# Performance work log

Hardware: AMD Instinct MI355X
Metric: run time of the kernel (lower is better)

## Reference

```python
import jax, jax.numpy as jnp
import numpy as np

B, LQ, D, H, NL, NP, DFF = 8, 1800, 256, 8, 4, 4, 1024
DH = D // H
SHAPES = np.array([[100, 150], [50, 75], [25, 38], [13, 19]], dtype=np.int64)
LIN = int((SHAPES[:, 0] * SHAPES[:, 1]).sum())
QN, QP = -8.0, 7.0  # 4-bit signed LSQ


def lsq(w, alpha):
    """LSQ weight quantization (per-tensor scale, STE round/grad-scale)."""
    g = 1.0 / jnp.sqrt(w.size * QP)
    a = alpha * g + jax.lax.stop_gradient(alpha - alpha * g)  # grad-scaled alpha
    wn = jnp.clip(w / a, QN, QP)
    wq = wn + jax.lax.stop_gradient(jnp.round(wn) - wn)       # round with STE
    return wq * a


def linear_q(x, w, b, a):
    return x @ lsq(w, a).T + b


def layer_norm(x, g, b, eps=1e-5):
    m = x.mean(-1, keepdims=True)
    v = ((x - m) ** 2).mean(-1, keepdims=True)
    return (x - m) / jnp.sqrt(v + eps) * g + b


def setup_inputs():
    key = jax.random.key(0)
    ks = list(jax.random.split(key, 20))

    def nrm(i, shape, s=0.02):
        return jax.random.normal(ks[i], shape, jnp.float32) * s

    def alpha(w):
        return 2.0 * jnp.mean(jnp.abs(w)) / jnp.sqrt(QP)

    qW, kW, vW, oW = nrm(0, (D, D)), nrm(1, (D, D)), nrm(2, (D, D)), nrm(3, (D, D))
    val_W = nrm(4, (D, D))
    off_W = nrm(5, (H * NL * NP * 2, D))
    aw_W = nrm(6, (H * NL * NP, D))
    out_W = nrm(7, (D, D))
    W1, W2 = nrm(8, (DFF, D)), nrm(9, (D, DFF))
    lsi = np.concatenate([[0], np.cumsum(SHAPES[:, 0] * SHAPES[:, 1])[:-1]]).astype(np.int64)
    z = jnp.zeros
    return dict(
        tgt=nrm(10, (B, LQ, D), 1.0),
        query_pos=nrm(11, (B, LQ, D), 1.0),
        reference_points=jax.random.uniform(ks[12], (B, LQ, NL, 2), jnp.float32),
        src=nrm(13, (B, LIN, D), 1.0),
        qW=qW, qb=z(D), kW=kW, kb=z(D), vW=vW, vb=z(D), oW=oW, ob=z(D),
        a_q=alpha(qW), a_k=alpha(kW), a_v=alpha(vW), a_o=alpha(oW),
        val_W=val_W, val_b=z(D), a_val=alpha(val_W),
        off_W=off_W, off_b=z(H * NL * NP * 2),
        aw_W=aw_W, aw_b=z(H * NL * NP),
        out_W=out_W, out_b=z(D), a_out=alpha(out_W),
        W1=W1, b1=z(DFF), a_w1=alpha(W1),
        W2=W2, b2=z(D), a_w2=alpha(W2),
        ln1_g=jnp.ones(D), ln1_b=z(D),
        ln2_g=jnp.ones(D), ln2_b=z(D),
        ln3_g=jnp.ones(D), ln3_b=z(D),
        src_spatial_shapes=jnp.asarray(SHAPES),
        level_start_index=jnp.asarray(lsi),
        src_padding_mask=jnp.zeros((B, LIN), dtype=bool),
    )


def reference(tgt, query_pos, reference_points, src,
              qW, qb, kW, kb, vW, vb, oW, ob, a_q, a_k, a_v, a_o,
              val_W, val_b, a_val, off_W, off_b, aw_W, aw_b, out_W, out_b, a_out,
              W1, b1, a_w1, W2, b2, a_w2,
              ln1_g, ln1_b, ln2_g, ln2_b, ln3_g, ln3_b,
              src_spatial_shapes, level_start_index, src_padding_mask):
    shapes = np.asarray(src_spatial_shapes)  # static spatial shapes per level

    # ---- quantized self-attention (dropout = eval mode, i.e. identity) ----
    qk_in = tgt + query_pos
    q = linear_q(qk_in, qW, qb, a_q).reshape(B, LQ, H, DH)
    k = linear_q(qk_in, kW, kb, a_k).reshape(B, LQ, H, DH)
    v = linear_q(tgt, vW, vb, a_v).reshape(B, LQ, H, DH)
    scores = jnp.einsum('bqhd,bkhd->bhqk', q, k) / jnp.sqrt(jnp.float32(DH))
    p = jax.nn.softmax(scores, axis=-1)
    sa = jnp.einsum('bhqk,bkhd->bqhd', p, v).reshape(B, LQ, D)
    tgt = layer_norm(tgt + linear_q(sa, oW, ob, a_o), ln2_g, ln2_b)

    # ---- quantized multi-scale deformable cross-attention ----
    query = tgt + query_pos
    value = linear_q(src, val_W, val_b, a_val)
    value = jnp.where(src_padding_mask[..., None], 0.0, value)
    value = value.reshape(B, LIN, H, DH)
    offs = (query @ off_W.T + off_b).reshape(B, LQ, H, NL, NP, 2)
    aw = (query @ aw_W.T + aw_b).reshape(B, LQ, H, NL * NP)
    aw = jax.nn.softmax(aw, axis=-1).reshape(B, LQ, H, NL, NP)
    # offset normalizer is (W_l, H_l)
    norm = jnp.asarray(shapes[:, ::-1].astype(np.float32))  # [NL, 2]
    loc = reference_points[:, :, None, :, None, :] + offs / norm[None, None, None, :, None, :]

    bidx = jnp.arange(B)[:, None, None, None]
    hidx = jnp.arange(H)[None, None, :, None]
    acc = jnp.zeros((B, LQ, H, DH), jnp.float32)
    start = 0
    for l in range(NL):
        Hl, Wl = int(shapes[l, 0]), int(shapes[l, 1])
        v_l = jax.lax.dynamic_slice_in_dim(value, start, Hl * Wl, 1).reshape(B, Hl, Wl, H, DH)
        # grid_sample semantics: align_corners=False, zero padding
        x = loc[:, :, :, l, :, 0] * Wl - 0.5  # [B, LQ, H, NP]
        y = loc[:, :, :, l, :, 1] * Hl - 0.5
        x0 = jnp.floor(x); y0 = jnp.floor(y)
        x0i = x0.astype(jnp.int32); y0i = y0.astype(jnp.int32)
        wx1 = x - x0; wy1 = y - y0
        wx0 = 1.0 - wx1; wy0 = 1.0 - wy1

        def gather(yi, xi):
            valid = (yi >= 0) & (yi < Hl) & (xi >= 0) & (xi < Wl)
            yc = jnp.clip(yi, 0, Hl - 1); xc = jnp.clip(xi, 0, Wl - 1)
            g = v_l[bidx, yc, xc, hidx]  # [B, LQ, H, NP, DH]
            return g * valid[..., None]

        samp = (gather(y0i, x0i) * (wy0 * wx0)[..., None]
                + gather(y0i, x0i + 1) * (wy0 * wx1)[..., None]
                + gather(y0i + 1, x0i) * (wy1 * wx0)[..., None]
                + gather(y0i + 1, x0i + 1) * (wy1 * wx1)[..., None])
        acc = acc + (aw[:, :, :, l, :, None] * samp).sum(axis=3)
        start += Hl * Wl

    ca = linear_q(acc.reshape(B, LQ, D), out_W, out_b, a_out)
    tgt = layer_norm(tgt + ca, ln1_g, ln1_b)

    # ---- quantized FFN ----
    t2 = linear_q(jax.nn.relu(linear_q(tgt, W1, b1, a_w1)), W2, b2, a_w2)
    tgt = layer_norm(tgt + t2, ln3_g, ln3_b)
    return tgt
```

## Files before the change

kernel.cpp:

```cpp
#include <hip/hip_runtime.h>
#include <hip/hip_bf16.h>

static constexpr int B_   = 8;
static constexpr int LQ_  = 1800;
static constexpr int D_   = 256;
static constexpr int H_   = 8;
static constexpr int DFF_ = 1024;
static constexpr int LIN_ = 19947;
static constexpr int MQ_  = B_ * LQ_;
static constexpr int NELEM_ = MQ_ * D_;

#define CDIV(a, b) (((a) + (b) - 1) / (b))

typedef unsigned short u16;
typedef unsigned int   u32;
typedef unsigned long long u64;
typedef __attribute__((ext_vector_type(8))) __bf16 bf16x8;
typedef __attribute__((ext_vector_type(4))) float  f32x4;
typedef __attribute__((ext_vector_type(4))) u32    u32x4;

#if __has_builtin(__builtin_amdgcn_exp2f)
#define EXP2(x) __builtin_amdgcn_exp2f(x)
#else
#define EXP2(x) exp2f(x)
#endif

__device__ __forceinline__ u16 f2bf(float f) {
    union { __bf16 h; u16 u; } v; v.h = (__bf16)f; return v.u;
}
__device__ __forceinline__ float bf2f(u16 u) {
    union { u32 u; float f; } v; v.u = ((u32)u) << 16;
    return v.f;
}

__device__ __forceinline__ f32x4 mfma_bf16(bf16x8 a, bf16x8 b, f32x4 c) {
    return __builtin_amdgcn_mfma_f32_16x16x32_bf16(a, b, c, 0, 0, 0);
}

__device__ __forceinline__ void gload16(const void* g, void* l) {
    __builtin_amdgcn_global_load_lds(
        (const __attribute__((address_space(1))) void*)g,
        (__attribute__((address_space(3))) void*)l,
        16, 0, 0);
}

template <int N> __device__ __forceinline__ void waitvm() {
    if constexpr (N == 0) asm volatile("s_waitcnt vmcnt(0)" ::: "memory");
    else if constexpr (N == 3) asm volatile("s_waitcnt vmcnt(3)" ::: "memory");
    else if constexpr (N == 4) asm volatile("s_waitcnt vmcnt(4)" ::: "memory");
    else if constexpr (N == 5) asm volatile("s_waitcnt vmcnt(5)" ::: "memory");
    else if constexpr (N == 6) asm volatile("s_waitcnt vmcnt(6)" ::: "memory");
}

__global__ void k_prep(
    const float* __restrict__ qW,   const float* __restrict__ kW,
    const float* __restrict__ vW,   const float* __restrict__ oW,
    const float* __restrict__ valW, const float* __restrict__ outW,
    const float* __restrict__ W1,   const float* __restrict__ W2,
    const float* __restrict__ offW, const float* __restrict__ awW,
    const float* __restrict__ a_q,  const float* __restrict__ a_k,
    const float* __restrict__ a_v,  const float* __restrict__ a_o,
    const float* __restrict__ a_val,const float* __restrict__ a_out,
    const float* __restrict__ a_w1, const float* __restrict__ a_w2,
    const float* __restrict__ qb,   const float* __restrict__ kb,
    const float* __restrict__ off_b,const float* __restrict__ aw_b,
    u16* __restrict__ wout, float* __restrict__ bout)
{
    int i = blockIdx.x * 256 + threadIdx.x;
    auto q8 = [&](const float* w, const float* al, int off) {
        float a = al[0];
        float wn = fminf(fmaxf(w[off] / a, -8.f), 7.f);
        wout[i] = f2bf(rintf(wn) * a);
    };
    if      (i <   65536) q8(qW,   a_q,   i);
    else if (i <  131072) q8(kW,   a_k,   i -   65536);
    else if (i <  196608) q8(vW,   a_v,   i -  131072);
    else if (i <  262144) q8(oW,   a_o,   i -  196608);
    else if (i <  327680) q8(valW, a_val, i -  262144);
    else if (i <  393216) q8(outW, a_out, i -  327680);
    else if (i <  655360) q8(W1,   a_w1,  i -  393216);
    else if (i <  917504) q8(W2,   a_w2,  i -  655360);
    else if (i <  983040) wout[i] = f2bf(offW[i - 917504]);
    else if (i < 1015808) wout[i] = f2bf(awW[i - 983040]);
    else if (i < 1016320) { int j = i - 1015808; bout[j]       = (j < 256) ? qb[j]    : kb[j - 256];  }
    else if (i < 1016704) { int j = i - 1016320; bout[512 + j] = (j < 256) ? off_b[j] : aw_b[j - 256]; }
}

__global__ void k_tgtprep(const float* __restrict__ tgt, const float* __restrict__ qpos,
                          u16* __restrict__ A, u16* __restrict__ Bb, int n) {
    int i = blockIdx.x * blockDim.x + threadIdx.x;
    if (i < n) { float t = tgt[i]; A[i] = f2bf(t + qpos[i]); Bb[i] = f2bf(t); }
}

__global__ void k_addcvt2(const u16* __restrict__ a, const float* __restrict__ b,
                          u16* __restrict__ o, int n) {
    int i = blockIdx.x * blockDim.x + threadIdx.x;
    if (i < n) o[i] = f2bf(bf2f(a[i]) + b[i]);
}

__device__ __forceinline__ void storey(float* p, float v) { *p = v; }
__device__ __forceinline__ void storey(u16* p, float v)   { *p = f2bf(v); }

template <typename XT, typename OT, bool RELU, int BN>
__global__ __launch_bounds__(256) void k_gemm3(
    const XT* __restrict__ X, const u16* __restrict__ W,
    const float* __restrict__ bias, OT* __restrict__ Y,
    int M, int N, int K)
{
    constexpr int WN  = BN / 2;
    constexpr int NFR = WN / 16;
    constexpr bool XF32 = (sizeof(XT) == 4);
    constexpr int L = (XF32 ? 2 : 1) + BN / 64;
    constexpr int ASZ = 64 * 32 * (XF32 ? 2 : 1);
    constexpr int BSZ = BN * 32;
    __shared__ __align__(16) u16 As[2][ASZ];
    __shared__ __align__(16) u16 Bs[2][BSZ];

    const int tid = threadIdx.x;
    const int wave = tid >> 6, lane = tid & 63;
    const int wr = wave >> 1, wc = wave & 1;
    const int fr = lane & 15, fg = lane >> 4;
    const int bm = blockIdx.x * 64, bn = blockIdx.y * BN;

    f32x4 acc[2][NFR];
    #pragma unroll
    for (int m = 0; m < 2; ++m)
        #pragma unroll
        for (int n = 0; n < NFR; ++n) acc[m][n] = (f32x4){0.f, 0.f, 0.f, 0.f};

    auto stageA = [&](int buf, int kt) {
        if constexpr (!XF32) {
            int r = (wave << 4) + (lane >> 2);
            int grow = bm + r; if (grow > M - 1) grow = M - 1;
            int cs = (lane & 3) ^ ((lane >> 3) & 3);
            gload16((const u16*)X + (size_t)grow * K + (kt << 5) + (cs << 3),
                    &As[buf][wave * 512]);
        } else {
            float* Af = (float*)As[buf];
            #pragma unroll
            for (int t = 0; t < 2; ++t) {
                int r = (t << 5) + (wave << 3) + (lane >> 3);
                int grow = bm + r; if (grow > M - 1) grow = M - 1;
                int cs = (lane & 7) ^ ((lane >> 3) & 7);
                gload16((const float*)X + (size_t)grow * K + (kt << 5) + (cs << 2),
                        &Af[((t << 5) + (wave << 3)) * 32]);
            }
        }
    };
    auto stageB = [&](int buf, int kt) {
        #pragma unroll
        for (int t = 0; t < BN / 64; ++t) {
            int r = (t << 6) + (wave << 4) + (lane >> 2);
            int cs = (lane & 3) ^ ((lane >> 3) & 3);
            gload16(W + (size_t)(bn + r) * K + (kt << 5) + (cs << 3),
                    &Bs[buf][((t << 6) + (wave << 4)) * 32]);
        }
    };

    stageA(0, 0); stageB(0, 0);

    const int nk = K >> 5;
    int cur = 0;
    for (int kt = 0; kt < nk; ++kt) {
        if (kt + 1 < nk) {
            stageA(cur ^ 1, kt + 1); stageB(cur ^ 1, kt + 1);
            waitvm<L>();
        } else {
            waitvm<0>();
        }
        __builtin_amdgcn_s_barrier();

        bf16x8 af[2], bg[NFR];
        #pragma unroll
        for (int m = 0; m < 2; ++m) {
            int r = wr * 32 + m * 16 + fr;
            if constexpr (!XF32) {
                af[m] = *(const bf16x8*)&As[cur][r * 32 + ((fg ^ ((fr >> 1) & 3)) << 3)];
            } else {
                const float* Af = (const float*)As[cur];
                int s0 = (fg << 1) ^ (fr & 7);
                f32x4 x0 = *(const f32x4*)&Af[r * 32 + (s0 << 2)];
                f32x4 x1 = *(const f32x4*)&Af[r * 32 + ((s0 ^ 1) << 2)];
                #pragma unroll
                for (int j = 0; j < 4; ++j) {
                    af[m][j]     = (__bf16)x0[j];
                    af[m][4 + j] = (__bf16)x1[j];
                }
            }
        }
        #pragma unroll
        for (int n = 0; n < NFR; ++n) {
            int r = wc * WN + n * 16 + fr;
            bg[n] = *(const bf16x8*)&Bs[cur][r * 32 + ((fg ^ ((fr >> 1) & 3)) << 3)];
        }
        #pragma unroll
        for (int m = 0; m < 2; ++m)
            #pragma unroll
            for (int n = 0; n < NFR; ++n)
                acc[m][n] = mfma_bf16(af[m], bg[n], acc[m][n]);

        __builtin_amdgcn_s_barrier();
        cur ^= 1;
    }

    #pragma unroll
    for (int m = 0; m < 2; ++m) {
        #pragma unroll
        for (int i = 0; i < 4; ++i) {
            int grow = bm + wr * 32 + m * 16 + fg * 4 + i;
            if (grow >= M) continue;
            #pragma unroll
            for (int n = 0; n < NFR; ++n) {
                int gcol = bn + wc * WN + n * 16 + fr;
                float v = acc[m][n][i] + bias[gcol];
                if (RELU) v = fmaxf(v, 0.f);
                storey(Y + (size_t)grow * N + gcol, v);
            }
        }
    }
}

__global__ __launch_bounds__(256) void k_attn(
    const u16* __restrict__ QK, const u16* __restrict__ V, u16* __restrict__ O)
{
    __shared__ u16 Ks[128 * 40];
    __shared__ u16 Vt[32 * 136];
    const int b = blockIdx.z, h = blockIdx.y;
    const int q0 = blockIdx.x * 64;
    const int tid = threadIdx.x;
    const int wave = tid >> 6, lane = tid & 63;
    const int fr = lane & 15, fg = lane >> 4;
    constexpr float C2 = 0.25503486f;

    int qg = q0 + wave * 16 + fr; if (qg >= LQ_) qg = LQ_ - 1;
    bf16x8 qf;
    {
        bf16x8 qraw = *(const bf16x8*)&QK[((size_t)(b * LQ_ + qg)) * 512 + h * 32 + fg * 8];
        #pragma unroll
        for (int j = 0; j < 8; ++j) qf[j] = (__bf16)((float)qraw[j] * C2);
    }

    const bf16x8 ones = {(__bf16)1.f, (__bf16)1.f, (__bf16)1.f, (__bf16)1.f,
                         (__bf16)1.f, (__bf16)1.f, (__bf16)1.f, (__bf16)1.f};

    f32x4 o0 = (f32x4){0.f,0.f,0.f,0.f}, o1 = (f32x4){0.f,0.f,0.f,0.f};
    f32x4 lacc = (f32x4){0.f,0.f,0.f,0.f};

    const int kr = tid >> 1, kc = (tid & 1) * 16;
    const int vp = lane, vdh = wave * 8;
    const int cp = ((vp >> 4) << 4) | (((vp >> 1) & 3) << 2) | (((vp >> 3) & 1) << 1) | (vp & 1);

    for (int kb0 = 0; kb0 < LQ_; kb0 += 128) {
        const bool tail = (kb0 + 128 > LQ_);
        __syncthreads();
        {
            int kg = kb0 + kr; if (kg >= LQ_) kg = LQ_ - 1;
            const u16* kp = &QK[((size_t)(b * LQ_ + kg)) * 512 + 256 + h * 32 + kc];
            *(bf16x8*)&Ks[kr * 40 + kc]     = *(const bf16x8*)kp;
            *(bf16x8*)&Ks[kr * 40 + kc + 8] = *(const bf16x8*)(kp + 8);
            int v0 = kb0 + 2 * vp, v1 = v0 + 1;
            if (v0 >= LQ_) v0 = LQ_ - 1;
            if (v1 >= LQ_) v1 = LQ_ - 1;
            union { bf16x8 v; u16 s[8]; } va, vb2;
            va.v  = *(const bf16x8*)&V[((size_t)(b * LQ_ + v0)) * 256 + h * 32 + vdh];
            vb2.v = *(const bf16x8*)&V[((size_t)(b * LQ_ + v1)) * 256 + h * 32 + vdh];
            #pragma unroll
            for (int j = 0; j < 8; ++j)
                *(u32*)&Vt[(vdh + j) * 136 + 2 * cp] = (u32)va.s[j] | ((u32)vb2.s[j] << 16);
        }
        __syncthreads();

        u32x4 pq[4];
        #pragma unroll
        for (int f = 0; f < 8; ++f) {
            bf16x8 ka = *(const bf16x8*)&Ks[(f * 16 + fr) * 40 + fg * 8];
            f32x4 s = mfma_bf16(ka, qf, (f32x4){0.f,0.f,0.f,0.f});
            if (tail) {
                #pragma unroll
                for (int i = 0; i < 4; ++i)
                    if (kb0 + f * 16 + fg * 4 + i >= LQ_) s[i] = -3e38f;
            }
            float p0 = EXP2(s[0]), p1 = EXP2(s[1]);
            float p2 = EXP2(s[2]), p3 = EXP2(s[3]);
            union { __bf16 h[2]; u32 w; } c0, c1;
            c0.h[0] = (__bf16)p0; c0.h[1] = (__bf16)p1;
            c1.h[0] = (__bf16)p2; c1.h[1] = (__bf16)p3;
            pq[f >> 1][(f & 1) * 2 + 0] = c0.w;
            pq[f >> 1][(f & 1) * 2 + 1] = c1.w;
        }

        #pragma unroll
        for (int ks = 0; ks < 4; ++ks) {
            bf16x8 pb  = __builtin_bit_cast(bf16x8, pq[ks]);
            bf16x8 va0 = *(const bf16x8*)&Vt[fr * 136 + ks * 32 + fg * 8];
            bf16x8 va1 = *(const bf16x8*)&Vt[(16 + fr) * 136 + ks * 32 + fg * 8];
            o0 = mfma_bf16(va0, pb, o0);
            o1 = mfma_bf16(va1, pb, o1);
            lacc = mfma_bf16(ones, pb, lacc);
        }
    }

    float inv = 1.f / lacc[0];
    int qout = q0 + wave * 16 + fr;
    if (qout < LQ_) {
        size_t base = ((size_t)(b * LQ_ + qout)) * 256 + h * 32;
        #pragma unroll
        for (int i = 0; i < 4; ++i) {
            O[base + fg * 4 + i]      = f2bf(o0[i] * inv);
            O[base + 16 + fg * 4 + i] = f2bf(o1[i] * inv);
        }
    }
}

__device__ __forceinline__ float ldf(const float* p) { return *p; }
__device__ __forceinline__ float ldf(const u16* p)   { return bf2f(*p); }

template <typename RT, typename OT>
__global__ __launch_bounds__(256) void k_resln(
    const u16* __restrict__ X, const RT* __restrict__ R,
    const float* __restrict__ g, const float* __restrict__ bb,
    OT* __restrict__ O)
{
    const int row = blockIdx.x;
    const int d = threadIdx.x;
    const size_t off = (size_t)row * D_ + d;
    float v = ldf(R + off) + bf2f(X[off]);
    __shared__ float r1[4], r2[4];
    int lane = d & 63, wid = d >> 6;
    float s = v;
    #pragma unroll
    for (int o_ = 32; o_ >= 1; o_ >>= 1) s += __shfl_xor(s, o_);
    if (lane == 0) r1[wid] = s;
    __syncthreads();
    float mean = (r1[0] + r1[1] + r1[2] + r1[3]) * (1.f / 256.f);
    float dv = v - mean;
    float sq = dv * dv;
    #pragma unroll
    for (int o_ = 32; o_ >= 1; o_ >>= 1) sq += __shfl_xor(sq, o_);
    if (lane == 0) r2[wid] = sq;
    __syncthreads();
    float var = (r2[0] + r2[1] + r2[2] + r2[3]) * (1.f / 256.f);
    storey(O + off, dv / sqrtf(var + 1e-5f) * g[d] + bb[d]);
}

__global__ __launch_bounds__(256) void k_sample(
    const float* __restrict__ oaw,
    const u16* __restrict__ value, const float* __restrict__ refp,
    u16* __restrict__ acc_out)
{
    __shared__ u32 pts[2][128][8];
    const int t = threadIdx.x;
    const int bq0 = blockIdx.x * 2;
    const int b = bq0 / LQ_;

    constexpr int Hl[4] = {100, 50, 25, 13};
    constexpr int Wl[4] = {150, 75, 38, 19};
    constexpr int LS[4] = {0, 15000, 18750, 19700};

    {
        const int qsub = t >> 7;
        const int pt = t & 127;
        const int h = pt >> 4, lp = pt & 15;
        const int l = lp >> 2, p = lp & 3;
        const int bq = bq0 + qsub;

        float2 oxy = *(const float2*)&oaw[(size_t)bq * 384 + h * 32 + l * 8 + p * 2];
        float av = oaw[(size_t)bq * 384 + 256 + h * 16 + lp];
        float mx = av;
        #pragma unroll
        for (int s = 1; s < 16; s <<= 1) mx = fmaxf(mx, __shfl_xor(mx, s));
        float e = __expf(av - mx);
        float sum = e;
        #pragma unroll
        for (int s = 1; s < 16; s <<= 1) sum += __shfl_xor(sum, s);
        float a = e / sum;

        float2 rxy = *(const float2*)&refp[(size_t)bq * 8 + l * 2];
        const float Wf = (float)Wl[l], Hf = (float)Hl[l];
        float x = (rxy.x + oxy.x / Wf) * Wf - 0.5f;
        float y = (rxy.y + oxy.y / Hf) * Hf - 0.5f;
        float x0f = floorf(x), y0f = floorf(y);
        int x0 = (int)x0f, y0 = (int)y0f;
        float wx1 = x - x0f, wy1 = y - y0f;
        float wx0 = 1.f - wx1, wy0 = 1.f - wy1;

        u32 ov[4]; float wv[4];
        #pragma unroll
        for (int c = 0; c < 4; ++c) {
            int cy = c >> 1, cx = c & 1;
            int yi = y0 + cy, xi = x0 + cx;
            bool valid = (yi >= 0) && (yi < Hl[l]) && (xi >= 0) && (xi < Wl[l]);
            ov[c] = valid ? (u32)((LS[l] + yi * Wl[l] + xi) * 256 + h * 32) : 0u;
            float w = (cy ? wy1 : wy0) * (cx ? wx1 : wx0) * a;
            wv[c] = valid ? w : 0.f;
        }
        u32* dst = pts[qsub][lp * 8 + h];
        *(uint4*)dst = make_uint4(ov[0], ov[1], ov[2], ov[3]);
        float4 wq = make_float4(wv[0], wv[1], wv[2], wv[3]);
        *(float4*)(dst + 4) = wq;
    }
    __syncthreads();

    const int qsub = t >> 7;
    const int h = (t >> 4) & 7;
    const int dp = t & 15;
    const u16* vb = value + (size_t)b * LIN_ * 256 + 2 * dp;
    float a0 = 0.f, a1 = 0.f;
    #pragma unroll
    for (int i = 0; i < 16; ++i) {
        const u32* P = pts[qsub][i * 8 + h];
        uint4 o4 = *(const uint4*)P;
        float4 w4 = *(const float4*)(P + 4);
        u32 g;
        g = *(const u32*)&vb[o4.x]; a0 += w4.x * bf2f((u16)g); a1 += w4.x * bf2f((u16)(g >> 16));
        g = *(const u32*)&vb[o4.y]; a0 += w4.y * bf2f((u16)g); a1 += w4.y * bf2f((u16)(g >> 16));
        g = *(const u32*)&vb[o4.z]; a0 += w4.z * bf2f((u16)g); a1 += w4.z * bf2f((u16)(g >> 16));
        g = *(const u32*)&vb[o4.w]; a0 += w4.w * bf2f((u16)g); a1 += w4.w * bf2f((u16)(g >> 16));
    }
    const int bq = bq0 + qsub;
    u32 packed = (u32)f2bf(a0) | ((u32)f2bf(a1) << 16);
    *(u32*)&acc_out[(size_t)bq * 256 + h * 32 + 2 * dp] = packed;
}

extern "C" void kernel_launch(void* const* d_in, const int* in_sizes, int n_in,
                              void* d_out, int out_size, void* d_ws, size_t ws_size,
                              hipStream_t stream)
{
    (void)in_sizes; (void)n_in; (void)out_size; (void)ws_size;
    const float* tgt   = (const float*)d_in[0];
    const float* qpos  = (const float*)d_in[1];
    const float* refp  = (const float*)d_in[2];
    const float* src   = (const float*)d_in[3];
    const float* qW    = (const float*)d_in[4];
    const float* qb    = (const float*)d_in[5];
    const float* kW    = (const float*)d_in[6];
    const float* kb    = (const float*)d_in[7];
    const float* vW    = (const float*)d_in[8];
    const float* vb    = (const float*)d_in[9];
    const float* oW    = (const float*)d_in[10];
    const float* ob    = (const float*)d_in[11];
    const float* a_q   = (const float*)d_in[12];
    const float* a_k   = (const float*)d_in[13];
    const float* a_v   = (const float*)d_in[14];
    const float* a_o   = (const float*)d_in[15];
    const float* val_W = (const float*)d_in[16];
    const float* val_b = (const float*)d_in[17];
    const float* a_val = (const float*)d_in[18];
    const float* off_W = (const float*)d_in[19];
    const float* off_b = (const float*)d_in[20];
    const float* aw_W  = (const float*)d_in[21];
    const float* aw_b  = (const float*)d_in[22];
    const float* out_W = (const float*)d_in[23];
    const float* out_b = (const float*)d_in[24];
    const float* a_out = (const float*)d_in[25];
    const float* W1    = (const float*)d_in[26];
    const float* b1    = (const float*)d_in[27];
    const float* a_w1  = (const float*)d_in[28];
    const float* W2    = (const float*)d_in[29];
    const float* b2    = (const float*)d_in[30];
    const float* a_w2  = (const float*)d_in[31];
    const float* ln1_g = (const float*)d_in[32];
    const float* ln1_b = (const float*)d_in[33];
    const float* ln2_g = (const float*)d_in[34];
    const float* ln2_b = (const float*)d_in[35];
    const float* ln3_g = (const float*)d_in[36];
    const float* ln3_b = (const float*)d_in[37];

    u16* wbase = (u16*)d_ws;
    u16* wq_q  = wbase;
    u16* wq_v  = wbase + 131072;
    u16* wq_o  = wbase + 196608;
    u16* wq_vl = wbase + 262144;
    u16* wq_ot = wbase + 327680;
    u16* wq_1  = wbase + 393216;
    u16* wq_2  = wbase + 655360;
    u16* w_off = wbase + 917504;
    float* bfused = (float*)(wbase + 1015808);
    u16* bufA = (u16*)(bfused + 1024);
    u16* bufB = bufA + NELEM_;
    u16* bufC = bufB + NELEM_;
    u16* bufD = bufC + NELEM_;
    u16* bufE = bufD + NELEM_;
    float* oaw = (float*)(bufE + NELEM_);
    u16* valb  = (u16*)(oaw + (size_t)MQ_ * 384);

    const int TB = 256;
    const int MVAL = B_ * LIN_;
    const int GM = MQ_ / 64;
    const int GV = CDIV(MVAL, 64);

    k_prep<<<CDIV(1016704, TB), TB, 0, stream>>>(
        qW, kW, vW, oW, val_W, out_W, W1, W2, off_W, aw_W,
        a_q, a_k, a_v, a_o, a_val, a_out, a_w1, a_w2,
        qb, kb, off_b, aw_b, wbase, bfused);
    k_tgtprep<<<CDIV(NELEM_, TB), TB, 0, stream>>>(tgt, qpos, bufA, bufB, NELEM_);

    k_gemm3<u16, u16, false, 128><<<dim3(GM, 4), TB, 0, stream>>>(bufA, wq_q, bfused, bufC, MQ_, 512, 256);
    k_gemm3<u16, u16, false, 128><<<dim3(GM, 2), TB, 0, stream>>>(bufB, wq_v, vb, bufE, MQ_, 256, 256);
    k_attn<<<dim3(CDIV(LQ_,64), H_, B_), TB, 0, stream>>>(bufC, bufE, bufA);
    k_gemm3<u16, u16, false, 128><<<dim3(GM, 2), TB, 0, stream>>>(bufA, wq_o, ob, bufD, MQ_, 256, 256);
    k_resln<float, u16><<<MQ_, TB, 0, stream>>>(bufD, tgt, ln2_g, ln2_b, bufC);

    k_addcvt2<<<CDIV(NELEM_, TB), TB, 0, stream>>>(bufC, qpos, bufD, NELEM_);
    k_gemm3<float, u16, false, 256><<<dim3(GV, 1), TB, 0, stream>>>(src, wq_vl, val_b, valb, MVAL, 256, 256);
    k_gemm3<u16, float, false, 128><<<dim3(GM, 3), TB, 0, stream>>>(bufD, w_off, bfused + 512, oaw, MQ_, 384, 256);
    k_sample<<<MQ_ / 2, TB, 0, stream>>>(oaw, valb, refp, bufE);
    k_gemm3<u16, u16, false, 128><<<dim3(GM, 2), TB, 0, stream>>>(bufE, wq_ot, out_b, bufA, MQ_, 256, 256);
    k_resln<u16, u16><<<MQ_, TB, 0, stream>>>(bufA, bufC, ln1_g, ln1_b, bufB);

    u16* ffn1 = valb;
    k_gemm3<u16, u16, true , 128><<<dim3(GM, 8), TB, 0, stream>>>(bufB, wq_1, b1, ffn1, MQ_, 1024, 256);
    k_gemm3<u16, u16, false, 128><<<dim3(GM, 2), TB, 0, stream>>>(ffn1, wq_2, b2, bufD, MQ_, 256, 1024);
    k_resln<u16, float><<<MQ_, TB, 0, stream>>>(bufD, bufB, ln3_g, ln3_b, (float*)d_out);
}
```

Baseline: 340.3 us.

## Load GEMM A-operand directly into registers and make K a compile-time constant

The GEMM kernel is replaced by a variant that loads the A operand straight from global memory into registers in MFMA fragment layout, prefetched two k-steps ahead, so A no longer goes through LDS. Only B is staged in shared memory with double buffering. K is now a template parameter, which lets the k-loop fully unroll. The large fp32 value-projection GEMM uses 512-thread blocks. This removes LDS traffic and LDS reads for A, at the cost of uncoalesced per-lane global loads and higher register pressure.

```diff
diff --git a/kernel.cpp b/kernel.cpp
--- a/kernel.cpp
+++ b/kernel.cpp
@@ -46,11 +46,14 @@
 
 template <int N> __device__ __forceinline__ void waitvm() {
     if constexpr (N == 0) asm volatile("s_waitcnt vmcnt(0)" ::: "memory");
-    else if constexpr (N == 3) asm volatile("s_waitcnt vmcnt(3)" ::: "memory");
+    else if constexpr (N == 2) asm volatile("s_waitcnt vmcnt(2)" ::: "memory");
     else if constexpr (N == 4) asm volatile("s_waitcnt vmcnt(4)" ::: "memory");
-    else if constexpr (N == 5) asm volatile("s_waitcnt vmcnt(5)" ::: "memory");
     else if constexpr (N == 6) asm volatile("s_waitcnt vmcnt(6)" ::: "memory");
-}
+    else if constexpr (N == 8) asm volatile("s_waitcnt vmcnt(8)" ::: "memory");
+}
+
+__device__ __forceinline__ void storey(float* p, float v) { *p = v; }
+__device__ __forceinline__ void storey(u16* p, float v)   { *p = f2bf(v); }
 
 __global__ void k_prep(
     const float* __restrict__ qW,   const float* __restrict__ kW,
@@ -98,29 +101,57 @@
     if (i < n) o[i] = f2bf(bf2f(a[i]) + b[i]);
 }
 
-__device__ __forceinline__ void storey(float* p, float v) { *p = v; }
-__device__ __forceinline__ void storey(u16* p, float v)   { *p = f2bf(v); }
-
-template <typename XT, typename OT, bool RELU, int BN>
-__global__ __launch_bounds__(256) void k_gemm3(
+template <typename XT, typename OT, bool RELU, int BN, int KK, int NT>
+__global__ __launch_bounds__(NT) void k_gemm4(
     const XT* __restrict__ X, const u16* __restrict__ W,
     const float* __restrict__ bias, OT* __restrict__ Y,
-    int M, int N, int K)
+    int M, int N)
 {
-    constexpr int WN  = BN / 2;
-    constexpr int NFR = WN / 16;
     constexpr bool XF32 = (sizeof(XT) == 4);
-    constexpr int L = (XF32 ? 2 : 1) + BN / 64;
-    constexpr int ASZ = 64 * 32 * (XF32 ? 2 : 1);
-    constexpr int BSZ = BN * 32;
-    __shared__ __align__(16) u16 As[2][ASZ];
-    __shared__ __align__(16) u16 Bs[2][BSZ];
+    constexpr int WC   = NT / 128;
+    constexpr int NFR  = (BN / WC) / 16;
+    constexpr int NK   = KK / 32;
+    constexpr int NB   = (BN * 4) / NT;
+    constexpr int NA   = XF32 ? 4 : 2;
+    constexpr int WAIT_N = NA + NB;
+    constexpr int ROWS_PER_OP = NT / 4;
+
+    __shared__ __align__(16) u16 Bs[2][BN * 32];
 
     const int tid = threadIdx.x;
     const int wave = tid >> 6, lane = tid & 63;
-    const int wr = wave >> 1, wc = wave & 1;
+    const int wr = wave / WC, wc = wave % WC;
     const int fr = lane & 15, fg = lane >> 4;
     const int bm = blockIdx.x * 64, bn = blockIdx.y * BN;
+
+    int r0 = bm + wr * 32 + fr;      if (r0 > M - 1) r0 = M - 1;
+    int r1 = bm + wr * 32 + 16 + fr; if (r1 > M - 1) r1 = M - 1;
+    const XT* xp0 = X + (size_t)r0 * KK + fg * 8;
+    const XT* xp1 = X + (size_t)r1 * KK + fg * 8;
+
+    bf16x8 aH[2][2];
+    f32x4  aF[2][2][2];
+
+    auto loadA = [&](int kt, int s) {
+        if constexpr (!XF32) {
+            aH[s][0] = *(const bf16x8*)(xp0 + kt * 32);
+            aH[s][1] = *(const bf16x8*)(xp1 + kt * 32);
+        } else {
+            aF[s][0][0] = *(const f32x4*)(xp0 + kt * 32);
+            aF[s][0][1] = *(const f32x4*)(xp0 + kt * 32 + 4);
+            aF[s][1][0] = *(const f32x4*)(xp1 + kt * 32);
+            aF[s][1][1] = *(const f32x4*)(xp1 + kt * 32 + 4);
+        }
+    };
+    auto stageB = [&](int buf, int kt) {
+        #pragma unroll
+        for (int t = 0; t < NB; ++t) {
+            int r = t * ROWS_PER_OP + (wave << 4) + (lane >> 2);
+            int cs = (lane & 3) ^ ((lane >> 3) & 3);
+            gload16(W + (size_t)(bn + r) * KK + (kt << 5) + (cs << 3),
+                    &Bs[buf][(t * ROWS_PER_OP + (wave << 4)) * 32]);
+        }
+    };
 
     f32x4 acc[2][NFR];
     #pragma unroll
@@ -128,69 +159,35 @@
         #pragma unroll
         for (int n = 0; n < NFR; ++n) acc[m][n] = (f32x4){0.f, 0.f, 0.f, 0.f};
 
-    auto stageA = [&](int buf, int kt) {
+    loadA(0, 0); stageB(0, 0);
+    waitvm<WAIT_N>();
+    loadA(1, 1);
+
+    #pragma unroll
+    for (int kt = 0; kt < NK; ++kt) {
+        const int cur = kt & 1, s = kt & 1;
+        if (kt + 1 < NK) { stageB(cur ^ 1, kt + 1); waitvm<WAIT_N>(); }
+        else             { waitvm<0>(); }
+        __builtin_amdgcn_s_barrier();
+
+        bf16x8 af[2];
         if constexpr (!XF32) {
-            int r = (wave << 4) + (lane >> 2);
-            int grow = bm + r; if (grow > M - 1) grow = M - 1;
-            int cs = (lane & 3) ^ ((lane >> 3) & 3);
-            gload16((const u16*)X + (size_t)grow * K + (kt << 5) + (cs << 3),
-                    &As[buf][wave * 512]);
+            af[0] = aH[s][0]; af[1] = aH[s][1];
         } else {
-            float* Af = (float*)As[buf];
             #pragma unroll
-            for (int t = 0; t < 2; ++t) {
-                int r = (t << 5) + (wave << 3) + (lane >> 3);
-                int grow = bm + r; if (grow > M - 1) grow = M - 1;
-                int cs = (lane & 7) ^ ((lane >> 3) & 7);
-                gload16((const float*)X + (size_t)grow * K + (kt << 5) + (cs << 2),
-                        &Af[((t << 5) + (wave << 3)) * 32]);
-            }
-        }
-    };
-    auto stageB = [&](int buf, int kt) {
-        #pragma unroll
-        for (int t = 0; t < BN / 64; ++t) {
-            int r = (t << 6) + (wave << 4) + (lane >> 2);
-            int cs = (lane & 3) ^ ((lane >> 3) & 3);
-            gload16(W + (size_t)(bn + r) * K + (kt << 5) + (cs << 3),
-                    &Bs[buf][((t << 6) + (wave << 4)) * 32]);
-        }
-    };
-
-    stageA(0, 0); stageB(0, 0);
-
-    const int nk = K >> 5;
-    int cur = 0;
-    for (int kt = 0; kt < nk; ++kt) {
-        if (kt + 1 < nk) {
-            stageA(cur ^ 1, kt + 1); stageB(cur ^ 1, kt + 1);
-            waitvm<L>();
-        } else {
-            waitvm<0>();
-        }
-        __builtin_amdgcn_s_barrier();
-
-        bf16x8 af[2], bg[NFR];
-        #pragma unroll
-        for (int m = 0; m < 2; ++m) {
-            int r = wr * 32 + m * 16 + fr;
-            if constexpr (!XF32) {
-                af[m] = *(const bf16x8*)&As[cur][r * 32 + ((fg ^ ((fr >> 1) & 3)) << 3)];
-            } else {
-                const float* Af = (const float*)As[cur];
-                int s0 = (fg << 1) ^ (fr & 7);
-                f32x4 x0 = *(const f32x4*)&Af[r * 32 + (s0 << 2)];
-                f32x4 x1 = *(const f32x4*)&Af[r * 32 + ((s0 ^ 1) << 2)];
+            for (int m = 0; m < 2; ++m)
                 #pragma unroll
                 for (int j = 0; j < 4; ++j) {
-                    af[m][j]     = (__bf16)x0[j];
-                    af[m][4 + j] = (__bf16)x1[j];
+                    af[m][j]     = (__bf16)aF[s][m][0][j];
+                    af[m][4 + j] = (__bf16)aF[s][m][1][j];
                 }
-            }
-        }
+        }
+        if (kt + 2 < NK) loadA(kt + 2, s);
+
+        bf16x8 bg[NFR];
         #pragma unroll
         for (int n = 0; n < NFR; ++n) {
-            int r = wc * WN + n * 16 + fr;
+            int r = wc * (NFR * 16) + n * 16 + fr;
             bg[n] = *(const bf16x8*)&Bs[cur][r * 32 + ((fg ^ ((fr >> 1) & 3)) << 3)];
         }
         #pragma unroll
@@ -200,7 +197,6 @@
                 acc[m][n] = mfma_bf16(af[m], bg[n], acc[m][n]);
 
         __builtin_amdgcn_s_barrier();
-        cur ^= 1;
     }
 
     #pragma unroll
@@ -211,7 +207,7 @@
             if (grow >= M) continue;
             #pragma unroll
             for (int n = 0; n < NFR; ++n) {
-                int gcol = bn + wc * WN + n * 16 + fr;
+                int gcol = bn + wc * (NFR * 16) + n * 16 + fr;
                 float v = acc[m][n][i] + bias[gcol];
                 if (RELU) v = fmaxf(v, 0.f);
                 storey(Y + (size_t)grow * N + gcol, v);
@@ -495,21 +491,21 @@
         qb, kb, off_b, aw_b, wbase, bfused);
     k_tgtprep<<<CDIV(NELEM_, TB), TB, 0, stream>>>(tgt, qpos, bufA, bufB, NELEM_);
 
-    k_gemm3<u16, u16, false, 128><<<dim3(GM, 4), TB, 0, stream>>>(bufA, wq_q, bfused, bufC, MQ_, 512, 256);
-    k_gemm3<u16, u16, false, 128><<<dim3(GM, 2), TB, 0, stream>>>(bufB, wq_v, vb, bufE, MQ_, 256, 256);
+    k_gemm4<u16, u16, false, 128, 256, 256><<<dim3(GM, 4), 256, 0, stream>>>(bufA, wq_q, bfused, bufC, MQ_, 512);
+    k_gemm4<u16, u16, false, 128, 256, 256><<<dim3(GM, 2), 256, 0, stream>>>(bufB, wq_v, vb, bufE, MQ_, 256);
     k_attn<<<dim3(CDIV(LQ_,64), H_, B_), TB, 0, stream>>>(bufC, bufE, bufA);
-    k_gemm3<u16, u16, false, 128><<<dim3(GM, 2), TB, 0, stream>>>(bufA, wq_o, ob, bufD, MQ_, 256, 256);
+    k_gemm4<u16, u16, false, 128, 256, 256><<<dim3(GM, 2), 256, 0, stream>>>(bufA, wq_o, ob, bufD, MQ_, 256);
     k_resln<float, u16><<<MQ_, TB, 0, stream>>>(bufD, tgt, ln2_g, ln2_b, bufC);
 
     k_addcvt2<<<CDIV(NELEM_, TB), TB, 0, stream>>>(bufC, qpos, bufD, NELEM_);
-    k_gemm3<float, u16, false, 256><<<dim3(GV, 1), TB, 0, stream>>>(src, wq_vl, val_b, valb, MVAL, 256, 256);
-    k_gemm3<u16, float, false, 128><<<dim3(GM, 3), TB, 0, stream>>>(bufD, w_off, bfused + 512, oaw, MQ_, 384, 256);
+    k_gemm4<float, u16, false, 256, 256, 512><<<dim3(GV, 1), 512, 0, stream>>>(src, wq_vl, val_b, valb, MVAL, 256);
+    k_gemm4<u16, float, false, 128, 256, 256><<<dim3(GM, 3), 256, 0, stream>>>(bufD, w_off, bfused + 512, oaw, MQ_, 384);
     k_sample<<<MQ_ / 2, TB, 0, stream>>>(oaw, valb, refp, bufE);
-    k_gemm3<u16, u16, false, 128><<<dim3(GM, 2), TB, 0, stream>>>(bufE, wq_ot, out_b, bufA, MQ_, 256, 256);
+    k_gemm4<u16, u16, false, 128, 256, 256><<<dim3(GM, 2), 256, 0, stream>>>(bufE, wq_ot, out_b, bufA, MQ_, 256);
     k_resln<u16, u16><<<MQ_, TB, 0, stream>>>(bufA, bufC, ln1_g, ln1_b, bufB);
 
     u16* ffn1 = valb;
-    k_gemm3<u16, u16, true , 128><<<dim3(GM, 8), TB, 0, stream>>>(bufB, wq_1, b1, ffn1, MQ_, 1024, 256);
-    k_gemm3<u16, u16, false, 128><<<dim3(GM, 2), TB, 0, stream>>>(ffn1, wq_2, b2, bufD, MQ_, 256, 1024);
+    k_gemm4<u16, u16, true , 128, 256,  256><<<dim3(GM, 8), 256, 0, stream>>>(bufB, wq_1, b1, ffn1, MQ_, 1024);
+    k_gemm4<u16, u16, false, 128, 1024, 256><<<dim3(GM, 2), 256, 0, stream>>>(ffn1, wq_2, b2, bufD, MQ_, 256);
     k_resln<u16, float><<<MQ_, TB, 0, stream>>>(bufD, bufB, ln3_g, ln3_b, (float*)d_out);
 }
```

New measurement: 400.2 us. 1.18x slower.
